# Optimization experiments

Hardware: AMD Instinct MI355X
Metric: run time of the kernel (lower is better)

## Reference

```python
import jax, jax.numpy as jnp
import numpy as np

N = 4096
RANK = 4
B = 2048
DT = 1.0
TAU = 1.0
ALPHA = float(np.sqrt(np.pi) / 2.0)  # erf slope so phi'(0)=1


def setup_inputs() -> dict:
    key = jax.random.key(0)
    k1, k2, k3, k4, k5, k6 = jax.random.split(key, 6)
    return {
        "x_t": jax.random.normal(k1, (1, B), dtype=jnp.float32),
        "h": jax.random.normal(k2, (N, B), dtype=jnp.float32),
        "m": jax.random.normal(k3, (N, 1), dtype=jnp.float32),
        "u": jax.random.normal(k4, (N, RANK), dtype=jnp.float32),
        "v": jax.random.normal(k5, (N, RANK), dtype=jnp.float32),
        "z": jax.random.normal(k6, (N, 1), dtype=jnp.float32),
    }


def reference(x_t, h, m, u, v, z):
    # phi(h) = erf(alpha * h)
    phi_h = jax.lax.erf(ALPHA * h)                      # [N, B]
    # W @ phi_h with W = (1/N) u v^T, reassociated to exploit low rank
    # (mathematically identical to materializing W)
    wph = (u @ (v.T @ phi_h)) / N                       # [N, B]
    h_update = wph + m @ x_t                            # [N, B]
    h_new = h + (DT / TAU) * (-h + h_update)            # [N, B]
    y = (z.T @ phi_h) / N                               # [1, B]
    return (y, h_new)
```

## Files before the change

kernel.cpp:

```cpp
#include <hip/hip_runtime.h>
#include <math.h>

#define N 4096
#define B 2048
#define RANK 4
#define ALPHA 0.8862269254527580f
#define INV_N (1.0f / 4096.0f)

#define TR 64
#define TC 256
#define NSPLIT (N / TR)
#define CSTRIPES (B / TC)
#define PLANE (5 * B)
#define RPB3 4

typedef float vf4 __attribute__((ext_vector_type(4)));

__device__ __forceinline__ float erf_fast(float t) {
  const float A = 0.140012288f;
  const float FP = 1.2732395447f;
  float t2 = t * t;
  float num = fmaf(A, t2, FP);
  float den = fmaf(A, t2, 1.0f);
  float r = t2 * num * __builtin_amdgcn_rcpf(den);
  float e = __expf(-r);
  float s = __builtin_amdgcn_sqrtf(fmaxf(1.0f - e, 0.0f));
  return copysignf(s, t);
}

__global__ __launch_bounds__(512) void k_phi_part(
    const float* __restrict__ h, const float* __restrict__ v,
    const float* __restrict__ z, float* __restrict__ partials) {
  __shared__ __align__(16) float red[5][8][TC];
  const int tid = threadIdx.x;
  const int l = tid & 63;
  const int g = tid >> 6;
  const int rg = blockIdx.x >> 3;
  const int cs = blockIdx.x & 7;
  const int r0 = rg * TR + g * 8;
  const int c0 = cs * TC;

  vf4 a0 = {0.f, 0.f, 0.f, 0.f};
  vf4 a1 = a0, a2 = a0, a3 = a0, a4 = a0;

  const float* hp = h + (size_t)r0 * B + c0 + l * 4;
#pragma unroll
  for (int r = 0; r < 8; ++r) {
    const vf4 hv = *(const vf4*)(hp + (size_t)r * B);
    vf4 p;
    p.x = erf_fast(ALPHA * hv.x);
    p.y = erf_fast(ALPHA * hv.y);
    p.z = erf_fast(ALPHA * hv.z);
    p.w = erf_fast(ALPHA * hv.w);
    const int row = __builtin_amdgcn_readfirstlane(r0 + r);
    const float v0 = v[row * RANK + 0];
    const float v1 = v[row * RANK + 1];
    const float v2 = v[row * RANK + 2];
    const float v3 = v[row * RANK + 3];
    const float zr = z[row];
    a0.x = fmaf(v0, p.x, a0.x); a0.y = fmaf(v0, p.y, a0.y);
    a0.z = fmaf(v0, p.z, a0.z); a0.w = fmaf(v0, p.w, a0.w);
    a1.x = fmaf(v1, p.x, a1.x); a1.y = fmaf(v1, p.y, a1.y);
    a1.z = fmaf(v1, p.z, a1.z); a1.w = fmaf(v1, p.w, a1.w);
    a2.x = fmaf(v2, p.x, a2.x); a2.y = fmaf(v2, p.y, a2.y);
    a2.z = fmaf(v2, p.z, a2.z); a2.w = fmaf(v2, p.w, a2.w);
    a3.x = fmaf(v3, p.x, a3.x); a3.y = fmaf(v3, p.y, a3.y);
    a3.z = fmaf(v3, p.z, a3.z); a3.w = fmaf(v3, p.w, a3.w);
    a4.x = fmaf(zr, p.x, a4.x); a4.y = fmaf(zr, p.y, a4.y);
    a4.z = fmaf(zr, p.z, a4.z); a4.w = fmaf(zr, p.w, a4.w);
  }

  *(vf4*)&red[0][g][l * 4] = a0;
  *(vf4*)&red[1][g][l * 4] = a1;
  *(vf4*)&red[2][g][l * 4] = a2;
  *(vf4*)&red[3][g][l * 4] = a3;
  *(vf4*)&red[4][g][l * 4] = a4;
  __syncthreads();

  for (int o = tid; o < 5 * TC; o += 512) {
    const int p = o >> 8;
    const int c = o & (TC - 1);
    float s = 0.f;
#pragma unroll
    for (int g2 = 0; g2 < 8; ++g2) s += red[p][g2][c];
    partials[(size_t)rg * PLANE + p * B + c0 + c] = s;
  }
}

__global__ __launch_bounds__(256) void k_reduce_final(
    const float* __restrict__ partials, float* __restrict__ sfin,
    float* __restrict__ y) {
  const int o4 = (blockIdx.x * 256 + threadIdx.x) * 4;
  const float* pp = partials + o4;
  vf4 s = {0.f, 0.f, 0.f, 0.f};
#pragma unroll 8
  for (int sp = 0; sp < NSPLIT; ++sp)
    s += *(const vf4*)(pp + (size_t)sp * PLANE);
  if (o4 < RANK * B) {
    *(vf4*)(sfin + o4) = s;
  } else {
    s *= INV_N;
    *(vf4*)(y + (o4 - RANK * B)) = s;
  }
}

__global__ __launch_bounds__(256) void k_update(
    const float* __restrict__ sfin, const float* __restrict__ u,
    const float* __restrict__ m, const float* __restrict__ x,
    float* __restrict__ hnew) {
  const int tid = threadIdx.x;
  const int row0 = blockIdx.x * RPB3;
  const int c0 = tid * 4;

  const vf4 sA0 = *(const vf4*)(sfin + 0 * B + c0);
  const vf4 sA1 = *(const vf4*)(sfin + 1 * B + c0);
  const vf4 sA2 = *(const vf4*)(sfin + 2 * B + c0);
  const vf4 sA3 = *(const vf4*)(sfin + 3 * B + c0);
  const vf4 xa  = *(const vf4*)(x + c0);
  const vf4 sB0 = *(const vf4*)(sfin + 0 * B + c0 + 1024);
  const vf4 sB1 = *(const vf4*)(sfin + 1 * B + c0 + 1024);
  const vf4 sB2 = *(const vf4*)(sfin + 2 * B + c0 + 1024);
  const vf4 sB3 = *(const vf4*)(sfin + 3 * B + c0 + 1024);
  const vf4 xb  = *(const vf4*)(x + c0 + 1024);

  float* op = hnew + (size_t)row0 * B + c0;
#pragma unroll
  for (int i = 0; i < RPB3; ++i) {
    const int n = row0 + i;
    const vf4 uv = *(const vf4*)(u + (size_t)n * RANK);
    const float mv = m[n];
    vf4 oA, oB;
    oA.x = fmaf(mv, xa.x,
                (sA0.x * uv.x + sA1.x * uv.y + sA2.x * uv.z + sA3.x * uv.w) * INV_N);
    oA.y = fmaf(mv, xa.y,
                (sA0.y * uv.x + sA1.y * uv.y + sA2.y * uv.z + sA3.y * uv.w) * INV_N);
    oA.z = fmaf(mv, xa.z,
                (sA0.z * uv.x + sA1.z * uv.y + sA2.z * uv.z + sA3.z * uv.w) * INV_N);
    oA.w = fmaf(mv, xa.w,
                (sA0.w * uv.x + sA1.w * uv.y + sA2.w * uv.z + sA3.w * uv.w) * INV_N);
    oB.x = fmaf(mv, xb.x,
                (sB0.x * uv.x + sB1.x * uv.y + sB2.x * uv.z + sB3.x * uv.w) * INV_N);
    oB.y = fmaf(mv, xb.y,
                (sB0.y * uv.x + sB1.y * uv.y + sB2.y * uv.z + sB3.y * uv.w) * INV_N);
    oB.z = fmaf(mv, xb.z,
                (sB0.z * uv.x + sB1.z * uv.y + sB2.z * uv.z + sB3.z * uv.w) * INV_N);
    oB.w = fmaf(mv, xb.w,
                (sB0.w * uv.x + sB1.w * uv.y + sB2.w * uv.z + sB3.w * uv.w) * INV_N);
    __builtin_nontemporal_store(oA, (vf4*)(op + (size_t)i * B));
    __builtin_nontemporal_store(oB, (vf4*)(op + (size_t)i * B + 1024));
  }
}

extern "C" void kernel_launch(void* const* d_in, const int* in_sizes, int n_in,
                              void* d_out, int out_size, void* d_ws,
                              size_t ws_size, hipStream_t stream) {
  const float* x = (const float*)d_in[0];
  const float* h = (const float*)d_in[1];
  const float* m = (const float*)d_in[2];
  const float* u = (const float*)d_in[3];
  const float* v = (const float*)d_in[4];
  const float* z = (const float*)d_in[5];

  float* y = (float*)d_out;
  float* hnew = (float*)d_out + B;

  float* partials = (float*)d_ws;
  float* sfin = partials + (size_t)NSPLIT * PLANE;

  k_phi_part<<<NSPLIT * CSTRIPES, 512, 0, stream>>>(h, v, z, partials);
  k_reduce_final<<<PLANE / 1024, 256, 0, stream>>>(partials, sfin, y);
  k_update<<<N / RPB3, 256, 0, stream>>>(sfin, u, m, x, hnew);
}
```

Measured before the change: 105.2 us.

## Fuse final partial reduction into phi kernel via last-block atomic ticket

Removes the separate reduction kernel. Each phi block takes an atomic ticket per column stripe after writing its partials, and the last block of that stripe reduces all row-group partials into sfin and y. A memset is added to reset the counters, so one kernel launch is replaced by a memset node. The final reduction is also done by only 8 blocks instead of being spread across many.

```diff
diff --git a/kernel.cpp b/kernel.cpp
--- a/kernel.cpp
+++ b/kernel.cpp
@@ -11,6 +11,7 @@
 #define TC 256
 #define NSPLIT (N / TR)
 #define CSTRIPES (B / TC)
+#define NBLK (NSPLIT * CSTRIPES)
 #define PLANE (5 * B)
 #define RPB3 4
 
@@ -28,10 +29,13 @@
   return copysignf(s, t);
 }
 
-__global__ __launch_bounds__(512) void k_phi_part(
+__global__ __launch_bounds__(512) void k_phi_fin(
     const float* __restrict__ h, const float* __restrict__ v,
-    const float* __restrict__ z, float* __restrict__ partials) {
+    const float* __restrict__ z, float* __restrict__ partials,
+    float* __restrict__ sfin, float* __restrict__ y,
+    unsigned int* __restrict__ cnt) {
   __shared__ __align__(16) float red[5][8][TC];
+  __shared__ unsigned int sticket;
   const int tid = threadIdx.x;
   const int l = tid & 63;
   const int g = tid >> 6;
@@ -85,22 +89,34 @@
     for (int g2 = 0; g2 < 8; ++g2) s += red[p][g2][c];
     partials[(size_t)rg * PLANE + p * B + c0 + c] = s;
   }
-}
 
-__global__ __launch_bounds__(256) void k_reduce_final(
-    const float* __restrict__ partials, float* __restrict__ sfin,
-    float* __restrict__ y) {
-  const int o4 = (blockIdx.x * 256 + threadIdx.x) * 4;
-  const float* pp = partials + o4;
-  vf4 s = {0.f, 0.f, 0.f, 0.f};
-#pragma unroll 8
-  for (int sp = 0; sp < NSPLIT; ++sp)
-    s += *(const vf4*)(pp + (size_t)sp * PLANE);
-  if (o4 < RANK * B) {
-    *(vf4*)(sfin + o4) = s;
-  } else {
-    s *= INV_N;
-    *(vf4*)(y + (o4 - RANK * B)) = s;
+  __threadfence();
+  __syncthreads();
+  if (tid == 0) sticket = atomicAdd(&cnt[cs], 1u);
+  __syncthreads();
+  if (sticket != NSPLIT - 1) return;
+
+  __threadfence();
+#pragma unroll
+  for (int k = 0; k < 5; ++k) {
+    const float* pp = partials + (size_t)(g * 8) * PLANE + k * B + c0 + l * 4;
+    vf4 s = {0.f, 0.f, 0.f, 0.f};
+#pragma unroll
+    for (int sp = 0; sp < 8; ++sp)
+      s += *(const vf4*)(pp + (size_t)sp * PLANE);
+    *(vf4*)&red[k][g][l * 4] = s;
+  }
+  __syncthreads();
+  for (int o = tid; o < 5 * TC; o += 512) {
+    const int p = o >> 8;
+    const int c = o & (TC - 1);
+    float s = 0.f;
+#pragma unroll
+    for (int g2 = 0; g2 < 8; ++g2) s += red[p][g2][c];
+    if (p < RANK)
+      sfin[p * B + c0 + c] = s;
+    else
+      y[c0 + c] = s * INV_N;
   }
 }
 
@@ -166,8 +182,9 @@
 
   float* partials = (float*)d_ws;
   float* sfin = partials + (size_t)NSPLIT * PLANE;
+  unsigned int* cnt = (unsigned int*)(sfin + RANK * B);
 
-  k_phi_part<<<NSPLIT * CSTRIPES, 512, 0, stream>>>(h, v, z, partials);
-  k_reduce_final<<<PLANE / 1024, 256, 0, stream>>>(partials, sfin, y);
+  hipMemsetAsync(cnt, 0, CSTRIPES * sizeof(unsigned int), stream);
+  k_phi_fin<<<NBLK, 512, 0, stream>>>(h, v, z, partials, sfin, y, cnt);
   k_update<<<N / RPB3, 256, 0, stream>>>(sfin, u, m, x, hnew);
 }
```

New measurement: 178.6 us. +69.7%, slower.

## Fuse final reduction into update kernel and reduce row splits to sixteen

Applied to the files above, without the earlier changes.

The phi/partial-sum kernel now runs 256 blocks of 1024 threads, each covering 256 rows by 128 columns. That cuts the number of row-split partial planes from 64 to 16. The separate reduce kernel is gone: each update block re-reduces the 16 partial planes for its 256-column stripe into shared memory and then writes h_new directly. This removes one kernel launch and the sfin round trip. In exchange, partials are read redundantly by every row-group block, and the first kernel has fewer, larger blocks, which lowers parallelism.

```diff
diff --git a/kernel.cpp b/kernel.cpp
--- a/kernel.cpp
+++ b/kernel.cpp
@@ -7,12 +7,8 @@
 #define ALPHA 0.8862269254527580f
 #define INV_N (1.0f / 4096.0f)
 
-#define TR 64
-#define TC 256
-#define NSPLIT (N / TR)
-#define CSTRIPES (B / TC)
+#define NSPLIT 16
 #define PLANE (5 * B)
-#define RPB3 4
 
 typedef float vf4 __attribute__((ext_vector_type(4)));
 
@@ -28,126 +24,138 @@
   return copysignf(s, t);
 }
 
-__global__ __launch_bounds__(512) void k_phi_part(
+__global__ __launch_bounds__(1024) void k_phi_part(
     const float* __restrict__ h, const float* __restrict__ v,
     const float* __restrict__ z, float* __restrict__ partials) {
-  __shared__ __align__(16) float red[5][8][TC];
+  __shared__ __align__(16) float red[5][16][2][128];
   const int tid = threadIdx.x;
   const int l = tid & 63;
-  const int g = tid >> 6;
-  const int rg = blockIdx.x >> 3;
-  const int cs = blockIdx.x & 7;
-  const int r0 = rg * TR + g * 8;
-  const int c0 = cs * TC;
+  const int w = tid >> 6;
+  const int rg = blockIdx.x >> 4;
+  const int cs = blockIdx.x & 15;
+  const int hf = l >> 5;
+  const int lc = (l & 31) * 4;
+  const int c0 = cs * 128;
+  const int rbase = rg * 256 + w * 16 + hf;
 
   vf4 a0 = {0.f, 0.f, 0.f, 0.f};
   vf4 a1 = a0, a2 = a0, a3 = a0, a4 = a0;
 
-  const float* hp = h + (size_t)r0 * B + c0 + l * 4;
+  const float* hp = h + (size_t)rbase * B + c0 + lc;
 #pragma unroll
-  for (int r = 0; r < 8; ++r) {
-    const vf4 hv = *(const vf4*)(hp + (size_t)r * B);
+  for (int i = 0; i < 8; ++i) {
+    const int row = rbase + 2 * i;
+    const vf4 hv = *(const vf4*)(hp + (size_t)(2 * i) * B);
+    const vf4 vv = *(const vf4*)(v + (size_t)row * RANK);
+    const float zr = z[row];
     vf4 p;
     p.x = erf_fast(ALPHA * hv.x);
     p.y = erf_fast(ALPHA * hv.y);
     p.z = erf_fast(ALPHA * hv.z);
     p.w = erf_fast(ALPHA * hv.w);
-    const int row = __builtin_amdgcn_readfirstlane(r0 + r);
-    const float v0 = v[row * RANK + 0];
-    const float v1 = v[row * RANK + 1];
-    const float v2 = v[row * RANK + 2];
-    const float v3 = v[row * RANK + 3];
-    const float zr = z[row];
-    a0.x = fmaf(v0, p.x, a0.x); a0.y = fmaf(v0, p.y, a0.y);
-    a0.z = fmaf(v0, p.z, a0.z); a0.w = fmaf(v0, p.w, a0.w);
-    a1.x = fmaf(v1, p.x, a1.x); a1.y = fmaf(v1, p.y, a1.y);
-    a1.z = fmaf(v1, p.z, a1.z); a1.w = fmaf(v1, p.w, a1.w);
-    a2.x = fmaf(v2, p.x, a2.x); a2.y = fmaf(v2, p.y, a2.y);
-    a2.z = fmaf(v2, p.z, a2.z); a2.w = fmaf(v2, p.w, a2.w);
-    a3.x = fmaf(v3, p.x, a3.x); a3.y = fmaf(v3, p.y, a3.y);
-    a3.z = fmaf(v3, p.z, a3.z); a3.w = fmaf(v3, p.w, a3.w);
+    a0.x = fmaf(vv.x, p.x, a0.x); a0.y = fmaf(vv.x, p.y, a0.y);
+    a0.z = fmaf(vv.x, p.z, a0.z); a0.w = fmaf(vv.x, p.w, a0.w);
+    a1.x = fmaf(vv.y, p.x, a1.x); a1.y = fmaf(vv.y, p.y, a1.y);
+    a1.z = fmaf(vv.y, p.z, a1.z); a1.w = fmaf(vv.y, p.w, a1.w);
+    a2.x = fmaf(vv.z, p.x, a2.x); a2.y = fmaf(vv.z, p.y, a2.y);
+    a2.z = fmaf(vv.z, p.z, a2.z); a2.w = fmaf(vv.z, p.w, a2.w);
+    a3.x = fmaf(vv.w, p.x, a3.x); a3.y = fmaf(vv.w, p.y, a3.y);
+    a3.z = fmaf(vv.w, p.z, a3.z); a3.w = fmaf(vv.w, p.w, a3.w);
     a4.x = fmaf(zr, p.x, a4.x); a4.y = fmaf(zr, p.y, a4.y);
     a4.z = fmaf(zr, p.z, a4.z); a4.w = fmaf(zr, p.w, a4.w);
   }
 
-  *(vf4*)&red[0][g][l * 4] = a0;
-  *(vf4*)&red[1][g][l * 4] = a1;
-  *(vf4*)&red[2][g][l * 4] = a2;
-  *(vf4*)&red[3][g][l * 4] = a3;
-  *(vf4*)&red[4][g][l * 4] = a4;
+  *(vf4*)&red[0][w][hf][lc] = a0;
+  *(vf4*)&red[1][w][hf][lc] = a1;
+  *(vf4*)&red[2][w][hf][lc] = a2;
+  *(vf4*)&red[3][w][hf][lc] = a3;
+  *(vf4*)&red[4][w][hf][lc] = a4;
   __syncthreads();
 
-  for (int o = tid; o < 5 * TC; o += 512) {
-    const int p = o >> 8;
-    const int c = o & (TC - 1);
+  if (tid < 5 * 128) {
+    const int p = tid >> 7;
+    const int c = tid & 127;
     float s = 0.f;
 #pragma unroll
-    for (int g2 = 0; g2 < 8; ++g2) s += red[p][g2][c];
+    for (int w2 = 0; w2 < 16; ++w2) {
+      s += red[p][w2][0][c];
+      s += red[p][w2][1][c];
+    }
     partials[(size_t)rg * PLANE + p * B + c0 + c] = s;
   }
 }
 
-__global__ __launch_bounds__(256) void k_reduce_final(
-    const float* __restrict__ partials, float* __restrict__ sfin,
-    float* __restrict__ y) {
-  const int o4 = (blockIdx.x * 256 + threadIdx.x) * 4;
-  const float* pp = partials + o4;
-  vf4 s = {0.f, 0.f, 0.f, 0.f};
-#pragma unroll 8
-  for (int sp = 0; sp < NSPLIT; ++sp)
-    s += *(const vf4*)(pp + (size_t)sp * PLANE);
-  if (o4 < RANK * B) {
-    *(vf4*)(sfin + o4) = s;
-  } else {
-    s *= INV_N;
-    *(vf4*)(y + (o4 - RANK * B)) = s;
+__global__ __launch_bounds__(512) void k_red_update(
+    const float* __restrict__ partials, const float* __restrict__ u,
+    const float* __restrict__ m, const float* __restrict__ x,
+    float* __restrict__ y, float* __restrict__ hnew) {
+  __shared__ __align__(16) float redA[4][2][256];
+  __shared__ __align__(16) float redY[2][256];
+  const int tid = threadIdx.x;
+  const int rg = blockIdx.x >> 3;
+  const int cs = blockIdx.x & 7;
+  const int c0 = cs * 256;
+
+  {
+    const int p = tid >> 7;
+    const int rem = tid & 127;
+    const int hf = rem >> 6;
+    const int cv = (rem & 63) * 4;
+    const float* pp = partials + (size_t)(hf * 8) * PLANE + p * B + c0 + cv;
+    vf4 sA = {0.f, 0.f, 0.f, 0.f};
+    vf4 sB = sA;
+#pragma unroll
+    for (int sp = 0; sp < 8; sp += 2) {
+      sA += *(const vf4*)(pp + (size_t)sp * PLANE);
+      sB += *(const vf4*)(pp + (size_t)(sp + 1) * PLANE);
+    }
+    sA += sB;
+    *(vf4*)&redA[p][hf][cv] = sA;
   }
-}
+  if (rg == 0 && tid < 128) {
+    const int hf = tid >> 6;
+    const int cv = (tid & 63) * 4;
+    const float* pp = partials + (size_t)(hf * 8) * PLANE + 4 * B + c0 + cv;
+    vf4 s = {0.f, 0.f, 0.f, 0.f};
+#pragma unroll
+    for (int sp = 0; sp < 8; ++sp)
+      s += *(const vf4*)(pp + (size_t)sp * PLANE);
+    *(vf4*)&redY[hf][cv] = s;
+  }
+  __syncthreads();
 
-__global__ __launch_bounds__(256) void k_update(
-    const float* __restrict__ sfin, const float* __restrict__ u,
-    const float* __restrict__ m, const float* __restrict__ x,
-    float* __restrict__ hnew) {
-  const int tid = threadIdx.x;
-  const int row0 = blockIdx.x * RPB3;
-  const int c0 = tid * 4;
+  if (rg == 0 && tid < 64) {
+    vf4 yy = *(const vf4*)&redY[0][tid * 4] + *(const vf4*)&redY[1][tid * 4];
+    yy *= INV_N;
+    *(vf4*)(y + c0 + tid * 4) = yy;
+  }
 
-  const vf4 sA0 = *(const vf4*)(sfin + 0 * B + c0);
-  const vf4 sA1 = *(const vf4*)(sfin + 1 * B + c0);
-  const vf4 sA2 = *(const vf4*)(sfin + 2 * B + c0);
-  const vf4 sA3 = *(const vf4*)(sfin + 3 * B + c0);
-  const vf4 xa  = *(const vf4*)(x + c0);
-  const vf4 sB0 = *(const vf4*)(sfin + 0 * B + c0 + 1024);
-  const vf4 sB1 = *(const vf4*)(sfin + 1 * B + c0 + 1024);
-  const vf4 sB2 = *(const vf4*)(sfin + 2 * B + c0 + 1024);
-  const vf4 sB3 = *(const vf4*)(sfin + 3 * B + c0 + 1024);
-  const vf4 xb  = *(const vf4*)(x + c0 + 1024);
+  const int g = tid >> 6;
+  const int l = tid & 63;
+  const int lc = l * 4;
+  const vf4 s0 = *(const vf4*)&redA[0][0][lc] + *(const vf4*)&redA[0][1][lc];
+  const vf4 s1 = *(const vf4*)&redA[1][0][lc] + *(const vf4*)&redA[1][1][lc];
+  const vf4 s2 = *(const vf4*)&redA[2][0][lc] + *(const vf4*)&redA[2][1][lc];
+  const vf4 s3 = *(const vf4*)&redA[3][0][lc] + *(const vf4*)&redA[3][1][lc];
+  const vf4 xa = *(const vf4*)(x + c0 + lc);
 
-  float* op = hnew + (size_t)row0 * B + c0;
+  const int r0 = rg * 64 + g * 8;
+  float* op = hnew + (size_t)r0 * B + c0 + lc;
 #pragma unroll
-  for (int i = 0; i < RPB3; ++i) {
-    const int n = row0 + i;
-    const vf4 uv = *(const vf4*)(u + (size_t)n * RANK);
-    const float mv = m[n];
-    vf4 oA, oB;
-    oA.x = fmaf(mv, xa.x,
-                (sA0.x * uv.x + sA1.x * uv.y + sA2.x * uv.z + sA3.x * uv.w) * INV_N);
-    oA.y = fmaf(mv, xa.y,
-                (sA0.y * uv.x + sA1.y * uv.y + sA2.y * uv.z + sA3.y * uv.w) * INV_N);
-    oA.z = fmaf(mv, xa.z,
-                (sA0.z * uv.x + sA1.z * uv.y + sA2.z * uv.z + sA3.z * uv.w) * INV_N);
-    oA.w = fmaf(mv, xa.w,
-                (sA0.w * uv.x + sA1.w * uv.y + sA2.w * uv.z + sA3.w * uv.w) * INV_N);
-    oB.x = fmaf(mv, xb.x,
-                (sB0.x * uv.x + sB1.x * uv.y + sB2.x * uv.z + sB3.x * uv.w) * INV_N);
-    oB.y = fmaf(mv, xb.y,
-                (sB0.y * uv.x + sB1.y * uv.y + sB2.y * uv.z + sB3.y * uv.w) * INV_N);
-    oB.z = fmaf(mv, xb.z,
-                (sB0.z * uv.x + sB1.z * uv.y + sB2.z * uv.z + sB3.z * uv.w) * INV_N);
-    oB.w = fmaf(mv, xb.w,
-                (sB0.w * uv.x + sB1.w * uv.y + sB2.w * uv.z + sB3.w * uv.w) * INV_N);
-    __builtin_nontemporal_store(oA, (vf4*)(op + (size_t)i * B));
-    __builtin_nontemporal_store(oB, (vf4*)(op + (size_t)i * B + 1024));
+  for (int r = 0; r < 8; ++r) {
+    const int row = __builtin_amdgcn_readfirstlane(r0 + r);
+    const vf4 uv = *(const vf4*)(u + (size_t)row * RANK);
+    const float mv = m[row];
+    vf4 o;
+    o.x = fmaf(mv, xa.x,
+               (s0.x * uv.x + s1.x * uv.y + s2.x * uv.z + s3.x * uv.w) * INV_N);
+    o.y = fmaf(mv, xa.y,
+               (s0.y * uv.x + s1.y * uv.y + s2.y * uv.z + s3.y * uv.w) * INV_N);
+    o.z = fmaf(mv, xa.z,
+               (s0.z * uv.x + s1.z * uv.y + s2.z * uv.z + s3.z * uv.w) * INV_N);
+    o.w = fmaf(mv, xa.w,
+               (s0.w * uv.x + s1.w * uv.y + s2.w * uv.z + s3.w * uv.w) * INV_N);
+    __builtin_nontemporal_store(o, (vf4*)(op + (size_t)r * B));
   }
 }
 
@@ -165,9 +173,7 @@
   float* hnew = (float*)d_out + B;
 
   float* partials = (float*)d_ws;
-  float* sfin = partials + (size_t)NSPLIT * PLANE;
 
-  k_phi_part<<<NSPLIT * CSTRIPES, 512, 0, stream>>>(h, v, z, partials);
-  k_reduce_final<<<PLANE / 1024, 256, 0, stream>>>(partials, sfin, y);
-  k_update<<<N / RPB3, 256, 0, stream>>>(sfin, u, m, x, hnew);
+  k_phi_part<<<256, 1024, 0, stream>>>(h, v, z, partials);
+  k_red_update<<<512, 512, 0, stream>>>(partials, u, m, x, y, hnew);
 }
```

Result: faster. 101.1 us (-3.9%).
